# Performance work log

Measured on AMD Instinct MI355X. Metric: run time of the kernel, lower is better.

Reference implementation:

```python
import jax, jax.numpy as jnp
import numpy as np

NB_HEAD = 16
SIZE_PER_HEAD = 64
D_MODEL = 1024
B, SQ, SK = 4, 2048, 2048


def setup_inputs() -> dict:
    key = jax.random.key(0)
    ks = jax.random.split(key, 8)
    Q_seq = jax.random.normal(ks[0], (B, SQ, D_MODEL), dtype=jnp.float32)
    K_seq = jax.random.normal(ks[1], (B, SK, D_MODEL), dtype=jnp.float32)
    V_seq = jax.random.normal(ks[2], (B, SK, D_MODEL), dtype=jnp.float32)
    Q_len = jax.random.randint(ks[3], (B, 1), 0, SQ, dtype=jnp.int32)
    V_len = jax.random.randint(ks[4], (B, 1), 0, SK, dtype=jnp.int32)
    out_dim = NB_HEAD * SIZE_PER_HEAD
    scale = float(np.sqrt(6.0 / (D_MODEL + out_dim)))  # glorot_uniform
    WQ = jax.random.uniform(ks[5], (D_MODEL, out_dim), jnp.float32, -scale, scale)
    WK = jax.random.uniform(ks[6], (D_MODEL, out_dim), jnp.float32, -scale, scale)
    WV = jax.random.uniform(ks[7], (D_MODEL, out_dim), jnp.float32, -scale, scale)
    return {"Q_seq": Q_seq, "K_seq": K_seq, "V_seq": V_seq,
            "Q_len": Q_len, "V_len": V_len, "WQ": WQ, "WK": WK, "WV": WV}


def reference(Q_seq, K_seq, V_seq, Q_len, V_len, WQ, WK, WV):
    b, sq, _ = Q_seq.shape
    sk = K_seq.shape[1]
    H, D = NB_HEAD, SIZE_PER_HEAD
    # projections -> [B, H, S, D]
    Q = (Q_seq @ WQ).reshape(b, sq, H, D).transpose(0, 2, 1, 3)
    K = (K_seq @ WK).reshape(b, sk, H, D).transpose(0, 2, 1, 3)
    V = (V_seq @ WV).reshape(b, sk, H, D).transpose(0, 2, 1, 3)
    # scaled dot-product scores [B, H, Sq, Sk]
    A = jnp.einsum('bhqd,bhkd->bhqk', Q, K) / jnp.float32(np.sqrt(D))
    # faithful to original Mask (no cumsum): masks ONLY the key position == V_len
    vmask = jax.nn.one_hot(V_len[:, 0], sk, dtype=A.dtype)  # [B, Sk]
    A = A - vmask[:, None, None, :] * jnp.float32(1e12)
    A = jax.nn.softmax(A, axis=-1)
    out = jnp.einsum('bhqk,bhkd->bhqd', A, V)
    out = out.transpose(0, 2, 1, 3).reshape(b, sq, H * D)
    # multiplicative mask: zeros ONLY the query position == Q_len
    qmask = 1.0 - jax.nn.one_hot(Q_len[:, 0], sq, dtype=out.dtype)  # [B, Sq]
    return out * qmask[:, :, None]
```

## Files before the change

kernel.cpp:

```cpp
#include <hip/hip_runtime.h>
#include <hip/hip_bf16.h>

typedef float f32x4 __attribute__((ext_vector_type(4)));
typedef float f32x16 __attribute__((ext_vector_type(16)));
typedef short bf16x8 __attribute__((ext_vector_type(8)));
typedef unsigned short u16;
typedef u16 u16x4 __attribute__((ext_vector_type(4)));
typedef u16 u16x8 __attribute__((ext_vector_type(8)));
typedef unsigned u32;
typedef unsigned u32x2 __attribute__((ext_vector_type(2)));

#define GLDS(gp, lp) __builtin_amdgcn_global_load_lds( \
    (const __attribute__((address_space(1))) void*)(gp), \
    (__attribute__((address_space(3))) void*)(lp), 16, 0, 0)

__device__ __forceinline__ u16 f2bf(float f) {
  union { float f; unsigned u; } v; v.f = f;
  unsigned r = v.u + 0x7fffu + ((v.u >> 16) & 1u);
  return (u16)(r >> 16);
}

__device__ __forceinline__ u32 cvtpk(float lo, float hi) {
  u32 r;
  asm("v_cvt_pk_bf16_f32 %0, %1, %2" : "=v"(r) : "v"(lo), "v"(hi));
  return r;
}

__global__ __launch_bounds__(256) void ktrans(const float* __restrict__ WQ,
                                              const float* __restrict__ WK,
                                              const float* __restrict__ WV,
                                              u16* __restrict__ Wt) {
  int z = blockIdx.z;
  const float* W = (z == 0) ? WQ : (z == 1) ? WK : WV;
  u16* o = Wt + (size_t)z * 1024 * 1024;
  float scale = (z == 0) ? 0.125f : 1.0f;
  __shared__ float tl[32][33];
  int tx = threadIdx.x & 31, ty = threadIdx.x >> 5;
  int ko = blockIdx.x * 32, no = blockIdx.y * 32;
#pragma unroll
  for (int i = 0; i < 32; i += 8)
    tl[ty + i][tx] = W[(size_t)(ko + ty + i) * 1024 + no + tx];
  __syncthreads();
#pragma unroll
  for (int i = 0; i < 32; i += 8)
    o[(size_t)(no + ty + i) * 1024 + ko + tx] = f2bf(tl[tx][ty + i] * scale);
}

__global__ __launch_bounds__(256, 2) void kproj(
    const float* __restrict__ A0, const float* __restrict__ A1, const float* __restrict__ A2,
    const u16* __restrict__ Wt, u16* __restrict__ Qw, u16* __restrict__ Kw, u16* __restrict__ Vt) {
  int z = blockIdx.z;
  const float* A = (z == 0) ? A0 : (z == 1) ? A1 : A2;
  const u16* Wz = Wt + (size_t)z * 1024 * 1024;
  __shared__ __align__(16) u16 lds[16384];
  int t = threadIdx.x;
  int lane = t & 63, w = t >> 6;
  int wm = (w >> 1) * 64, wn = (w & 1) * 64;
  int m0 = blockIdx.y * 128, n0 = blockIdx.x * 128;
  f32x4 acc[4][4];
#pragma unroll
  for (int i = 0; i < 4; ++i)
#pragma unroll
    for (int j = 0; j < 4; ++j) acc[i][j] = (f32x4){0.f, 0.f, 0.f, 0.f};

  int srow = t >> 3, sk8 = (t & 7) << 3;
  int lbw = (t >> 6) * 512;

  for (int k0 = 0; k0 < 1024; k0 += 64) {
    __syncthreads();
#pragma unroll
    for (int p = 0; p < 4; ++p) {
      int row = srow + p * 32;
      const u16* gp = Wz + (size_t)(n0 + row) * 1024 + k0 + (sk8 ^ ((row & 7) << 3));
      GLDS(gp, &lds[8192 + p * 2048 + lbw]);
    }
#pragma unroll
    for (int p = 0; p < 4; ++p) {
      int row = srow + p * 32;
      const float* ap = A + (size_t)(m0 + row) * 1024 + k0 + sk8;
      f32x4 v0 = *(const f32x4*)ap, v1 = *(const f32x4*)(ap + 4);
      union { u32 u[4]; u16x8 v; } pk;
      pk.u[0] = cvtpk(v0.x, v0.y); pk.u[1] = cvtpk(v0.z, v0.w);
      pk.u[2] = cvtpk(v1.x, v1.y); pk.u[3] = cvtpk(v1.z, v1.w);
      *(u16x8*)(&lds[row * 64 + (sk8 ^ ((row & 7) << 3))]) = pk.v;
    }
    __syncthreads();
#pragma unroll
    for (int kk = 0; kk < 64; kk += 32) {
      int ko8 = kk + ((lane >> 4) << 3);
      bf16x8 af[4], bfr[4];
#pragma unroll
      for (int mi = 0; mi < 4; ++mi) {
        int r = wm + mi * 16 + (lane & 15);
        af[mi] = *(const bf16x8*)(&lds[r * 64 + (ko8 ^ ((r & 7) << 3))]);
      }
#pragma unroll
      for (int ni = 0; ni < 4; ++ni) {
        int r = wn + ni * 16 + (lane & 15);
        bfr[ni] = *(const bf16x8*)(&lds[8192 + r * 64 + (ko8 ^ ((r & 7) << 3))]);
      }
#pragma unroll
      for (int mi = 0; mi < 4; ++mi)
#pragma unroll
        for (int ni = 0; ni < 4; ++ni)
          acc[mi][ni] = __builtin_amdgcn_mfma_f32_16x16x32_bf16(af[mi], bfr[ni], acc[mi][ni], 0, 0, 0);
    }
  }
  int bb = m0 >> 11;
  if (z < 2) {
    u16* o = (z == 0) ? Qw : Kw;
#pragma unroll
    for (int mi = 0; mi < 4; ++mi) {
      int m4 = m0 + wm + mi * 16 + ((lane >> 4) << 2);
      int s4 = m4 & 2047;
#pragma unroll
      for (int ni = 0; ni < 4; ++ni) {
        int n = n0 + wn + ni * 16 + (lane & 15);
        int hh = n >> 6, d = n & 63;
        u16* op = o + (((size_t)(bb * 16 + hh) * 2048 + s4) * 64 + d);
#pragma unroll
        for (int j = 0; j < 4; ++j) op[(size_t)j * 64] = f2bf(acc[mi][ni][j]);
      }
    }
  } else {
#pragma unroll
    for (int mi = 0; mi < 4; ++mi) {
      int m4 = m0 + wm + mi * 16 + ((lane >> 4) << 2);
      int s4 = m4 & 2047;
#pragma unroll
      for (int ni = 0; ni < 4; ++ni) {
        int n = n0 + wn + ni * 16 + (lane & 15);
        int hh = n >> 6, d = n & 63;
        u16x4 pv = {f2bf(acc[mi][ni][0]), f2bf(acc[mi][ni][1]),
                    f2bf(acc[mi][ni][2]), f2bf(acc[mi][ni][3])};
        *(u16x4*)(&Vt[((size_t)(bb * 16 + hh) * 64 + d) * 2048 + s4]) = pv;
      }
    }
  }
}

__global__ __launch_bounds__(512, 4) void kattn(
    const u16* __restrict__ Qw, const u16* __restrict__ Kw, const u16* __restrict__ Vt,
    const int* __restrict__ Qlen, const int* __restrict__ Vlen, float* __restrict__ out) {
  int fid = blockIdx.x;
  int bh = (fid & 7) * 8 + (fid >> 6);
  int qx = (fid >> 3) & 7;
  int b = bh >> 4, h = bh & 15;
  int q0 = qx * 256;
  int t = threadIdx.x, lane = t & 63, w = t >> 6, hi = lane >> 5, ln = lane & 31;
  __shared__ __align__(16) u16 smem[16384];
  const int qlen = Qlen[b], vlen = Vlen[b];

  const u16* Qp = Qw + ((size_t)bh * 2048 + q0 + w * 32 + ln) * 64;
  bf16x8 qf[4];
#pragma unroll
  for (int r = 0; r < 4; ++r) qf[r] = *(const bf16x8*)(Qp + r * 16 + hi * 8);

  int srow = t >> 3;
  int sks = (((t & 7) << 4) ^ ((srow & 7) << 4)) >> 1;
  const u16* gK = Kw + ((size_t)bh * 2048 + srow) * 64 + sks;
  const u16* gV = Vt + ((size_t)bh * 64 + srow) * 2048 + sks;
  int lbw = (t >> 6) * 512;

  GLDS(gK, &smem[lbw]);
  GLDS(gV, &smem[4096 + lbw]);

  float M = -1e30f, Lloc = 0.f;
  f32x16 o0, o1;
#pragma unroll
  for (int i = 0; i < 16; ++i) { o0[i] = 0.f; o1[i] = 0.f; }
  __syncthreads();

  for (int kt = 0; kt < 32; ++kt) {
    int qb = (kt & 1) * 8192;
    int nb = ((kt & 1) ^ 1) * 8192;
    if (kt < 31) {
      GLDS(gK + (size_t)(kt + 1) * 4096, &smem[nb + lbw]);
      GLDS(gV + (kt + 1) * 64, &smem[nb + 4096 + lbw]);
    }
    f32x16 sa[2];
#pragma unroll
    for (int kb = 0; kb < 2; ++kb)
#pragma unroll
      for (int i = 0; i < 16; ++i) sa[kb][i] = 0.f;
#pragma unroll
    for (int kb = 0; kb < 2; ++kb) {
      int row = kb * 32 + ln;
      int rs7 = (row & 7) << 4;
#pragma unroll
      for (int r = 0; r < 4; ++r) {
        int byt = row * 128 + ((r * 32 + hi * 16) ^ rs7);
        bf16x8 kf = *(const bf16x8*)(&smem[qb + (byt >> 1)]);
        sa[kb] = __builtin_amdgcn_mfma_f32_32x32x16_bf16(kf, qf[r], sa[kb], 0, 0, 0);
      }
    }
    if ((vlen >> 6) == kt) {
#pragma unroll
      for (int kb = 0; kb < 2; ++kb)
#pragma unroll
        for (int i = 0; i < 16; ++i) {
          int kv = (kt << 6) + kb * 32 + ((i & 3) + ((i >> 2) << 3)) + (hi << 2);
          if (kv == vlen) sa[kb][i] = -1e12f;
        }
    }
    float tmax = sa[0][0];
#pragma unroll
    for (int i = 1; i < 16; ++i) tmax = fmaxf(tmax, sa[0][i]);
#pragma unroll
    for (int i = 0; i < 16; ++i) tmax = fmaxf(tmax, sa[1][i]);
    tmax = fmaxf(tmax, __shfl_xor(tmax, 32, 64));
    if (!__all(tmax - M <= 8.f)) {
      float Mn = fmaxf(M, tmax);
      float al = __expf(M - Mn);
      M = Mn;
      Lloc *= al;
#pragma unroll
      for (int i = 0; i < 16; ++i) { o0[i] *= al; o1[i] *= al; }
    }
    float rs = 0.f;
#pragma unroll
    for (int kb = 0; kb < 2; ++kb)
#pragma unroll
      for (int i = 0; i < 16; ++i) {
        float p = __expf(sa[kb][i] - M);
        sa[kb][i] = p;
        rs += p;
      }
    Lloc += rs;
    bf16x8 pf[4];
#pragma unroll
    for (int kb = 0; kb < 2; ++kb)
#pragma unroll
      for (int f = 0; f < 2; ++f) {
        u32 a0 = cvtpk(sa[kb][8 * f + 0], sa[kb][8 * f + 1]);
        u32 b0 = cvtpk(sa[kb][8 * f + 4], sa[kb][8 * f + 5]);
        u32x2 r0 = __builtin_amdgcn_permlane32_swap(a0, b0, false, false);
        u32 a1 = cvtpk(sa[kb][8 * f + 2], sa[kb][8 * f + 3]);
        u32 b1 = cvtpk(sa[kb][8 * f + 6], sa[kb][8 * f + 7]);
        u32x2 r1 = __builtin_amdgcn_permlane32_swap(a1, b1, false, false);
        union { u32 u[4]; bf16x8 v; } uu;
        uu.u[0] = r0.x; uu.u[1] = r1.x; uu.u[2] = r0.y; uu.u[3] = r1.y;
        pf[kb * 2 + f] = uu.v;
      }
#pragma unroll
    for (int db = 0; db < 2; ++db) {
      int row = db * 32 + ln;
      int rs7 = (row & 7) << 4;
#pragma unroll
      for (int s4 = 0; s4 < 4; ++s4) {
        int byt = row * 128 + ((s4 * 32 + hi * 16) ^ rs7);
        bf16x8 vf = *(const bf16x8*)(&smem[qb + 4096 + (byt >> 1)]);
        if (db == 0) o0 = __builtin_amdgcn_mfma_f32_32x32x16_bf16(vf, pf[s4], o0, 0, 0, 0);
        else         o1 = __builtin_amdgcn_mfma_f32_32x32x16_bf16(vf, pf[s4], o1, 0, 0, 0);
      }
    }
    __syncthreads();
  }
  float Lt = Lloc + __shfl_xor(Lloc, 32, 64);
  int q = q0 + w * 32 + ln;
  float inv = (q == qlen) ? 0.f : 1.f / Lt;
  float* op = out + ((size_t)b * 2048 + q) * 1024 + h * 64;
#pragma unroll
  for (int g = 0; g < 4; ++g) {
    f32x4 v0 = {o0[4 * g + 0] * inv, o0[4 * g + 1] * inv, o0[4 * g + 2] * inv, o0[4 * g + 3] * inv};
    *(f32x4*)(op + g * 8 + hi * 4) = v0;
    f32x4 v1 = {o1[4 * g + 0] * inv, o1[4 * g + 1] * inv, o1[4 * g + 2] * inv, o1[4 * g + 3] * inv};
    *(f32x4*)(op + 32 + g * 8 + hi * 4) = v1;
  }
}

extern "C" void kernel_launch(void* const* d_in, const int* in_sizes, int n_in,
                              void* d_out, int out_size, void* d_ws, size_t ws_size,
                              hipStream_t stream) {
  (void)in_sizes; (void)n_in; (void)out_size; (void)ws_size;
  const float* Qs = (const float*)d_in[0];
  const float* Ks = (const float*)d_in[1];
  const float* Vs = (const float*)d_in[2];
  const int* Ql = (const int*)d_in[3];
  const int* Vl = (const int*)d_in[4];
  const float* WQ = (const float*)d_in[5];
  const float* WK = (const float*)d_in[6];
  const float* WV = (const float*)d_in[7];
  float* out = (float*)d_out;

  u16* Wt = (u16*)d_ws;
  u16* Qw = Wt + (size_t)3 * 1024 * 1024;
  u16* Kw = Qw + (size_t)8 * 1024 * 1024;
  u16* Vtw = Kw + (size_t)8 * 1024 * 1024;

  ktrans<<<dim3(32, 32, 3), 256, 0, stream>>>(WQ, WK, WV, Wt);
  kproj<<<dim3(8, 64, 3), 256, 0, stream>>>(Qs, Ks, Vs, Wt, Qw, Kw, Vtw);
  kattn<<<512, 512, 0, stream>>>(Qw, Kw, Vtw, Ql, Vl, out);
}
```

Measured before the change: 328.3 us.

## Pre-convert activations to bf16, split projection launches, use exp2 softmax

Activations are now converted to bf16 in a separate pass, so the projection GEMM can load both operands straight into LDS with global_load_lds instead of doing fp32 loads and conversions in its inner loop. The projection runs as three separate launches with a swizzled tile order and occupancy raised to 3 blocks. The 1/sqrt(d)*log2(e) factor is folded into WQ so attention can use exp2f, and the max and sum reductions are split into four independent chains. This adds extra kernel launches and an extra bf16 round trip through global memory for the activations, and the three projections no longer share one launch.

```diff
diff --git a/kernel.cpp b/kernel.cpp
--- a/kernel.cpp
+++ b/kernel.cpp
@@ -33,7 +33,7 @@
   int z = blockIdx.z;
   const float* W = (z == 0) ? WQ : (z == 1) ? WK : WV;
   u16* o = Wt + (size_t)z * 1024 * 1024;
-  float scale = (z == 0) ? 0.125f : 1.0f;
+  float scale = (z == 0) ? 0.18033688f : 1.0f;
   __shared__ float tl[32][33];
   int tx = threadIdx.x & 31, ty = threadIdx.x >> 5;
   int ko = blockIdx.x * 32, no = blockIdx.y * 32;
@@ -46,17 +46,30 @@
     o[(size_t)(no + ty + i) * 1024 + ko + tx] = f2bf(tl[tx][ty + i] * scale);
 }
 
-__global__ __launch_bounds__(256, 2) void kproj(
-    const float* __restrict__ A0, const float* __restrict__ A1, const float* __restrict__ A2,
-    const u16* __restrict__ Wt, u16* __restrict__ Qw, u16* __restrict__ Kw, u16* __restrict__ Vt) {
-  int z = blockIdx.z;
-  const float* A = (z == 0) ? A0 : (z == 1) ? A1 : A2;
-  const u16* Wz = Wt + (size_t)z * 1024 * 1024;
+__global__ __launch_bounds__(256) void kconv(const float* __restrict__ A, u16* __restrict__ Ab) {
+  int tid = blockIdx.x * 256 + threadIdx.x;
+  size_t base = (size_t)tid * 16;
+  const f32x4* p = (const f32x4*)(A + base);
+  f32x4 v0 = p[0], v1 = p[1], v2 = p[2], v3 = p[3];
+  union { u32 u[8]; u16x8 h[2]; } pk;
+  pk.u[0] = cvtpk(v0.x, v0.y); pk.u[1] = cvtpk(v0.z, v0.w);
+  pk.u[2] = cvtpk(v1.x, v1.y); pk.u[3] = cvtpk(v1.z, v1.w);
+  pk.u[4] = cvtpk(v2.x, v2.y); pk.u[5] = cvtpk(v2.z, v2.w);
+  pk.u[6] = cvtpk(v3.x, v3.y); pk.u[7] = cvtpk(v3.z, v3.w);
+  *(u16x8*)(Ab + base) = pk.h[0];
+  *(u16x8*)(Ab + base + 8) = pk.h[1];
+}
+
+__global__ __launch_bounds__(256, 3) void kproj(
+    const u16* __restrict__ Ab, const u16* __restrict__ Wz,
+    u16* __restrict__ O, int isV) {
   __shared__ __align__(16) u16 lds[16384];
-  int t = threadIdx.x;
-  int lane = t & 63, w = t >> 6;
+  int t = threadIdx.x, lane = t & 63, w = t >> 6;
   int wm = (w >> 1) * 64, wn = (w & 1) * 64;
-  int m0 = blockIdx.y * 128, n0 = blockIdx.x * 128;
+  int f = blockIdx.y * 8 + blockIdx.x;
+  int x_t = (f >> 3) & 7;
+  int y_t = (f & 7) | ((f >> 6) << 3);
+  int m0 = y_t * 128, n0 = x_t * 128;
   f32x4 acc[4][4];
 #pragma unroll
   for (int i = 0; i < 4; ++i)
@@ -64,26 +77,16 @@
     for (int j = 0; j < 4; ++j) acc[i][j] = (f32x4){0.f, 0.f, 0.f, 0.f};
 
   int srow = t >> 3, sk8 = (t & 7) << 3;
-  int lbw = (t >> 6) * 512;
+  int lbw = w * 512;
+  const u16* gA = Ab + (size_t)(m0 + srow) * 1024 + (sk8 ^ ((srow & 7) << 3));
+  const u16* gB = Wz + (size_t)(n0 + srow) * 1024 + (sk8 ^ ((srow & 7) << 3));
 
   for (int k0 = 0; k0 < 1024; k0 += 64) {
     __syncthreads();
 #pragma unroll
-    for (int p = 0; p < 4; ++p) {
-      int row = srow + p * 32;
-      const u16* gp = Wz + (size_t)(n0 + row) * 1024 + k0 + (sk8 ^ ((row & 7) << 3));
-      GLDS(gp, &lds[8192 + p * 2048 + lbw]);
-    }
-#pragma unroll
-    for (int p = 0; p < 4; ++p) {
-      int row = srow + p * 32;
-      const float* ap = A + (size_t)(m0 + row) * 1024 + k0 + sk8;
-      f32x4 v0 = *(const f32x4*)ap, v1 = *(const f32x4*)(ap + 4);
-      union { u32 u[4]; u16x8 v; } pk;
-      pk.u[0] = cvtpk(v0.x, v0.y); pk.u[1] = cvtpk(v0.z, v0.w);
-      pk.u[2] = cvtpk(v1.x, v1.y); pk.u[3] = cvtpk(v1.z, v1.w);
-      *(u16x8*)(&lds[row * 64 + (sk8 ^ ((row & 7) << 3))]) = pk.v;
-    }
+    for (int p = 0; p < 4; ++p) GLDS(gA + p * 32768 + k0, &lds[p * 2048 + lbw]);
+#pragma unroll
+    for (int p = 0; p < 4; ++p) GLDS(gB + p * 32768 + k0, &lds[8192 + p * 2048 + lbw]);
     __syncthreads();
 #pragma unroll
     for (int kk = 0; kk < 64; kk += 32) {
@@ -107,8 +110,7 @@
     }
   }
   int bb = m0 >> 11;
-  if (z < 2) {
-    u16* o = (z == 0) ? Qw : Kw;
+  if (!isV) {
 #pragma unroll
     for (int mi = 0; mi < 4; ++mi) {
       int m4 = m0 + wm + mi * 16 + ((lane >> 4) << 2);
@@ -117,7 +119,7 @@
       for (int ni = 0; ni < 4; ++ni) {
         int n = n0 + wn + ni * 16 + (lane & 15);
         int hh = n >> 6, d = n & 63;
-        u16* op = o + (((size_t)(bb * 16 + hh) * 2048 + s4) * 64 + d);
+        u16* op = O + (((size_t)(bb * 16 + hh) * 2048 + s4) * 64 + d);
 #pragma unroll
         for (int j = 0; j < 4; ++j) op[(size_t)j * 64] = f2bf(acc[mi][ni][j]);
       }
@@ -133,7 +135,7 @@
         int hh = n >> 6, d = n & 63;
         u16x4 pv = {f2bf(acc[mi][ni][0]), f2bf(acc[mi][ni][1]),
                     f2bf(acc[mi][ni][2]), f2bf(acc[mi][ni][3])};
-        *(u16x4*)(&Vt[((size_t)(bb * 16 + hh) * 64 + d) * 2048 + s4]) = pv;
+        *(u16x4*)(&O[((size_t)(bb * 16 + hh) * 64 + d) * 2048 + s4]) = pv;
       }
     }
   }
@@ -203,44 +205,52 @@
           if (kv == vlen) sa[kb][i] = -1e12f;
         }
     }
-    float tmax = sa[0][0];
-#pragma unroll
-    for (int i = 1; i < 16; ++i) tmax = fmaxf(tmax, sa[0][i]);
-#pragma unroll
-    for (int i = 0; i < 16; ++i) tmax = fmaxf(tmax, sa[1][i]);
+    float t0 = sa[0][0], t1 = sa[0][1], t2 = sa[0][2], t3 = sa[0][3];
+#pragma unroll
+    for (int i = 4; i < 16; i += 4) {
+      t0 = fmaxf(t0, sa[0][i]);     t1 = fmaxf(t1, sa[0][i + 1]);
+      t2 = fmaxf(t2, sa[0][i + 2]); t3 = fmaxf(t3, sa[0][i + 3]);
+    }
+#pragma unroll
+    for (int i = 0; i < 16; i += 4) {
+      t0 = fmaxf(t0, sa[1][i]);     t1 = fmaxf(t1, sa[1][i + 1]);
+      t2 = fmaxf(t2, sa[1][i + 2]); t3 = fmaxf(t3, sa[1][i + 3]);
+    }
+    float tmax = fmaxf(fmaxf(t0, t1), fmaxf(t2, t3));
     tmax = fmaxf(tmax, __shfl_xor(tmax, 32, 64));
-    if (!__all(tmax - M <= 8.f)) {
+    if (!__all(tmax - M <= 11.54f)) {
       float Mn = fmaxf(M, tmax);
-      float al = __expf(M - Mn);
+      float al = exp2f(M - Mn);
       M = Mn;
       Lloc *= al;
 #pragma unroll
       for (int i = 0; i < 16; ++i) { o0[i] *= al; o1[i] *= al; }
     }
-    float rs = 0.f;
+    float r0 = 0.f, r1 = 0.f, r2 = 0.f, r3 = 0.f;
 #pragma unroll
     for (int kb = 0; kb < 2; ++kb)
 #pragma unroll
-      for (int i = 0; i < 16; ++i) {
-        float p = __expf(sa[kb][i] - M);
-        sa[kb][i] = p;
-        rs += p;
-      }
-    Lloc += rs;
+      for (int i = 0; i < 16; i += 4) {
+        float p0 = exp2f(sa[kb][i] - M);     sa[kb][i] = p0;     r0 += p0;
+        float p1 = exp2f(sa[kb][i + 1] - M); sa[kb][i + 1] = p1; r1 += p1;
+        float p2 = exp2f(sa[kb][i + 2] - M); sa[kb][i + 2] = p2; r2 += p2;
+        float p3 = exp2f(sa[kb][i + 3] - M); sa[kb][i + 3] = p3; r3 += p3;
+      }
+    Lloc += (r0 + r1) + (r2 + r3);
     bf16x8 pf[4];
 #pragma unroll
     for (int kb = 0; kb < 2; ++kb)
 #pragma unroll
-      for (int f = 0; f < 2; ++f) {
-        u32 a0 = cvtpk(sa[kb][8 * f + 0], sa[kb][8 * f + 1]);
-        u32 b0 = cvtpk(sa[kb][8 * f + 4], sa[kb][8 * f + 5]);
-        u32x2 r0 = __builtin_amdgcn_permlane32_swap(a0, b0, false, false);
-        u32 a1 = cvtpk(sa[kb][8 * f + 2], sa[kb][8 * f + 3]);
-        u32 b1 = cvtpk(sa[kb][8 * f + 6], sa[kb][8 * f + 7]);
-        u32x2 r1 = __builtin_amdgcn_permlane32_swap(a1, b1, false, false);
+      for (int ff = 0; ff < 2; ++ff) {
+        u32 a0 = cvtpk(sa[kb][8 * ff + 0], sa[kb][8 * ff + 1]);
+        u32 b0 = cvtpk(sa[kb][8 * ff + 4], sa[kb][8 * ff + 5]);
+        u32x2 q0v = __builtin_amdgcn_permlane32_swap(a0, b0, false, false);
+        u32 a1 = cvtpk(sa[kb][8 * ff + 2], sa[kb][8 * ff + 3]);
+        u32 b1 = cvtpk(sa[kb][8 * ff + 6], sa[kb][8 * ff + 7]);
+        u32x2 q1v = __builtin_amdgcn_permlane32_swap(a1, b1, false, false);
         union { u32 u[4]; bf16x8 v; } uu;
-        uu.u[0] = r0.x; uu.u[1] = r1.x; uu.u[2] = r0.y; uu.u[3] = r1.y;
-        pf[kb * 2 + f] = uu.v;
+        uu.u[0] = q0v.x; uu.u[1] = q1v.x; uu.u[2] = q0v.y; uu.u[3] = q1v.y;
+        pf[kb * 2 + ff] = uu.v;
       }
 #pragma unroll
     for (int db = 0; db < 2; ++db) {
@@ -283,12 +293,19 @@
   const float* WV = (const float*)d_in[7];
   float* out = (float*)d_out;
 
+  const size_t M1 = 1024 * 1024;
   u16* Wt = (u16*)d_ws;
-  u16* Qw = Wt + (size_t)3 * 1024 * 1024;
-  u16* Kw = Qw + (size_t)8 * 1024 * 1024;
-  u16* Vtw = Kw + (size_t)8 * 1024 * 1024;
+  u16* Qw = Wt + 3 * M1;
+  u16* Kw = Qw + 8 * M1;
+  u16* Vtw = Kw + 8 * M1;
+  u16* Ab = Vtw + 8 * M1;
 
   ktrans<<<dim3(32, 32, 3), 256, 0, stream>>>(WQ, WK, WV, Wt);
-  kproj<<<dim3(8, 64, 3), 256, 0, stream>>>(Qs, Ks, Vs, Wt, Qw, Kw, Vtw);
+  kconv<<<2048, 256, 0, stream>>>(Qs, Ab);
+  kproj<<<dim3(8, 64), 256, 0, stream>>>(Ab, Wt, Qw, 0);
+  kconv<<<2048, 256, 0, stream>>>(Ks, Ab);
+  kproj<<<dim3(8, 64), 256, 0, stream>>>(Ab, Wt + M1, Kw, 0);
+  kconv<<<2048, 256, 0, stream>>>(Vs, Ab);
+  kproj<<<dim3(8, 64), 256, 0, stream>>>(Ab, Wt + 2 * M1, Vtw, 1);
   kattn<<<512, 512, 0, stream>>>(Qw, Kw, Vtw, Ql, Vl, out);
 }
```

Measured after the change: 333.8 us. No clear change (+1.7%).
